# Kernel tuning notes

Hardware: AMD Instinct MI355X
Metric: run time of the kernel (lower is better)

Reference implementation:

```python
import jax, jax.numpy as jnp
import numpy as np

S, N, L = 64, 256, 32
LANG_ID, D = 256, 128  # lang_od == pc_od == D
K = 16  # k; effective neighbors = k+1


def _mlp(x, w1, b1, w2, b2):
    return jnp.maximum(x @ w1 + b1, 0.0) @ w2 + b2


def setup_inputs() -> dict:
    key = jax.random.key(0)
    ks = jax.random.split(key, 16)
    def lin(k, fi, fo):
        return jax.random.normal(k, (fi, fo), jnp.float32) / np.sqrt(fi)
    inp = {
        "feat": jax.random.normal(ks[0], (S, N, D), jnp.float32),
        "coord": jax.random.normal(ks[1], (S, N, 3), jnp.float32),
        "lang_feat": jax.random.normal(ks[2], (S, L, LANG_ID), jnp.float32),
        "lang_len": jax.random.randint(ks[3], (S,), 1, L + 1),
        "rel_w1": lin(ks[4], 10, D), "rel_b1": jnp.zeros((D,), jnp.float32),
        "rel_w2": lin(ks[5], D, D), "rel_b2": jnp.zeros((D,), jnp.float32),
        "lang_w1": lin(ks[6], LANG_ID, D), "lang_b1": jnp.zeros((D,), jnp.float32),
        "lang_w2": lin(ks[7], D, D), "lang_b2": jnp.zeros((D,), jnp.float32),
        "feat_w1": lin(ks[8], D, D), "feat_b1": jnp.zeros((D,), jnp.float32),
        "feat_w2": lin(ks[9], D, D), "feat_b2": jnp.zeros((D,), jnp.float32),
    }
    return inp


def reference(feat, coord, lang_feat, lang_len,
              rel_w1, rel_b1, rel_w2, rel_b2,
              lang_w1, lang_b1, lang_w2, lang_b2,
              feat_w1, feat_b1, feat_w2, feat_b2):
    num_sen, num_obj, _ = feat.shape
    k1 = min(K, num_obj - 1) + 1  # k+1 neighbors including self
    # pairwise squared distances [S,N,N]
    d = ((coord[:, None, :, :] - coord[:, :, None, :]) ** 2).sum(-1)
    # k+1 nearest neighbors (smallest distance)
    _, idx = jax.lax.top_k(-d, k1)  # [S,N,k1]
    b = jnp.arange(num_sen)[:, None, None]
    coord_nb = coord[b, idx]  # [S,N,k1,3]
    coord_ctr = jnp.broadcast_to(coord[:, :, None, :], coord_nb.shape)
    rel_coord = coord_nb - coord_ctr
    dist = jnp.sqrt((rel_coord ** 2).sum(-1, keepdims=True))
    rel = jnp.concatenate([coord_nb, coord_ctr, rel_coord, dist], -1)  # [S,N,k1,10]
    rel = _mlp(rel, rel_w1, rel_b1, rel_w2, rel_b2)  # [S,N,k1,D]
    lang = _mlp(lang_feat, lang_w1, lang_b1, lang_w2, lang_b2)  # [S,L,D]
    f = _mlp(feat, feat_w1, feat_b1, feat_w2, feat_b2)  # [S,N,D]
    f_nb = f[b, idx]  # [S,N,k1,D]
    # attention of each (obj, neighbor) over language tokens
    attn = jnp.einsum('snkd,sld->snkl', f_nb, lang)
    attn = jax.nn.softmax(attn, axis=-1)
    max_len = lang_feat.shape[1]
    mask = (jnp.arange(max_len)[None, :] < lang_len[:, None]).astype(f.dtype)  # [S,L]
    attn = attn * mask[:, None, None, :]
    attn = attn / (attn.sum(-1, keepdims=True) + 1e-7)
    ins = jnp.einsum('snkl,sld->snkd', attn, lang)  # [S,N,k1,D]
    out = (f_nb * ins * rel).sum(2) + f  # [S,N,D]
    score = out.sum(-1)  # [S,N]
    return out, score
```

## Files before the change

### kernel.cpp

```cpp
#include <hip/hip_runtime.h>
#include <math.h>

#define S_ 64
#define N_ 256
#define L_ 32
#define D_ 128
#define LID_ 256
#define K1_ 17
#define CH_ 32
#define NW_ 8

typedef __attribute__((ext_vector_type(8))) short short8;
typedef __attribute__((ext_vector_type(4))) float f32x4;

__device__ __forceinline__ unsigned short f2bf(float f) {
  unsigned int u = __float_as_uint(f);
  u += 0x7fffu + ((u >> 16) & 1u);
  return (unsigned short)(u >> 16);
}


__global__ __launch_bounds__(256) void tar_prep_kernel(
    const float* __restrict__ rw1, const float* __restrict__ rb1,
    const float* __restrict__ rw2, const float* __restrict__ fw1,
    const float* __restrict__ fw2, const float* __restrict__ lw1,
    const float* __restrict__ lw2, unsigned short* __restrict__ w1T,
    unsigned short* __restrict__ w2T, unsigned short* __restrict__ fw1T,
    unsigned short* __restrict__ fw2T, unsigned short* __restrict__ lw1T,
    unsigned short* __restrict__ lw2T) {
  int t = blockIdx.x * 256 + threadIdx.x;
  {
    int k = t >> 7, n = t & 127;
    lw1T[(size_t)n * 256 + k] = f2bf(lw1[(size_t)k * 128 + n]);
  }
  if (t < 16384) {
    int k = t >> 7, n = t & 127;
    int slot =
        32 * (k >> 5) + 8 * ((k & 15) >> 2) + 4 * ((k >> 4) & 1) + (k & 3);
    w2T[(size_t)n * 128 + slot] = f2bf(rw2[(size_t)k * 128 + n]);
    fw1T[(size_t)n * 128 + k] = f2bf(fw1[(size_t)k * 128 + n]);
    fw2T[(size_t)n * 128 + k] = f2bf(fw2[(size_t)k * 128 + n]);
    lw2T[(size_t)n * 128 + k] = f2bf(lw2[(size_t)k * 128 + n]);
  }
  if (t < 2048) {
    int n2 = t >> 4, k2 = t & 15;
    unsigned short v = 0;
    if (k2 < 10) v = f2bf(rw1[(size_t)k2 * 128 + n2]);
    else if (k2 == 10) v = f2bf(rb1[n2]);
    w1T[(size_t)n2 * 16 + k2] = v;
  }
}

#define KNN_NB 1024
#define LANG_NB 32
#define FM_NB 256
__global__ __launch_bounds__(256, 4) void tar_prologue(
    const float* __restrict__ coord, int* __restrict__ idx_out,
    const float* __restrict__ lx, const unsigned short* __restrict__ lw1T,
    const float* __restrict__ lb1, const unsigned short* __restrict__ lw2T,
    const float* __restrict__ lb2, unsigned short* __restrict__ lang_bf,
    unsigned short* __restrict__ langT_bf, const float* __restrict__ fx,
    const unsigned short* __restrict__ fw1T, const float* __restrict__ fb1,
    const unsigned short* __restrict__ fw2T, const float* __restrict__ fb2,
    float* __restrict__ f_out, unsigned short* __restrict__ f_bf) {
  __shared__ __align__(16) char uarena[51200];
  int bid = blockIdx.x;
  int tid = threadIdx.x;

  if (bid < KNN_NB) {
    int wv = tid >> 6, l = tid & 63, grp = l >> 4, ln16 = l & 15;
    int obj = bid * 16 + wv * 4 + grp;
    int s = obj >> 8, n = obj & 255;
    const float* cs = coord + (size_t)s * N_ * 3;
    float cx = cs[n * 3 + 0], cy = cs[n * 3 + 1], cz = cs[n * 3 + 2];
    unsigned kd[16];
#pragma unroll
    for (int q = 0; q < 16; ++q) {
      int j = ln16 + q * 16;
      float dx = cs[j * 3 + 0] - cx;
      float dy = cs[j * 3 + 1] - cy;
      float dz = cs[j * 3 + 2] - cz;
      kd[q] = __float_as_uint(dx * dx + dy * dy + dz * dz);
    }
    for (int k = 0; k < K1_; ++k) {
      unsigned m = kd[0];
#pragma unroll
      for (int q = 1; q < 16; ++q) m = min(m, kd[q]);
      int bq = 0;
#pragma unroll
      for (int q = 15; q >= 0; --q)
        if (kd[q] == m) bq = q;
      int bj = ln16 + bq * 16;
      unsigned bm = m;
#pragma unroll
      for (int off = 1; off <= 8; off <<= 1) {
        unsigned om = __shfl_xor(bm, off);
        int oj = __shfl_xor(bj, off);
        if (om < bm || (om == bm && oj < bj)) { bm = om; bj = oj; }
      }
#pragma unroll
      for (int q = 0; q < 16; ++q)
        if (ln16 + q * 16 == bj) kd[q] = 0xFFFFFFFFu;
      if (ln16 == 0) idx_out[(size_t)obj * K1_ + k] = bj;
    }
  } else if (bid < KNN_NB + LANG_NB) {
    unsigned short* x_s = (unsigned short*)uarena;
    unsigned short* h_s = (unsigned short*)(uarena + 33792);
    int base = (bid - KNN_NB) * 64;
    int w = tid >> 6, l = tid & 63, g = l >> 4, ln = l & 15;
    for (int i = tid; i < 64 * 64; i += 256) {
      int row = i >> 6, c4 = (i & 63) * 4;
      float4 v = *(const float4*)&lx[(size_t)(base + row) * LID_ + c4];
      unsigned short* dst = &x_s[row * 264 + c4];
      dst[0] = f2bf(v.x); dst[1] = f2bf(v.y);
      dst[2] = f2bf(v.z); dst[3] = f2bf(v.w);
    }
    __syncthreads();
    float b1v[8], b2v[8];
#pragma unroll
    for (int nt = 0; nt < 8; ++nt) {
      b1v[nt] = lb1[nt * 16 + ln];
      b2v[nt] = lb2[nt * 16 + ln];
    }
    short8 a1[8];
#pragma unroll
    for (int kk = 0; kk < 8; ++kk)
      a1[kk] = *(const short8*)&x_s[(w * 16 + ln) * 264 + kk * 32 + g * 8];
    unsigned short* hw = &h_s[w * 16 * 136];
#pragma unroll
    for (int nt = 0; nt < 8; ++nt) {
      f32x4 acc = {b1v[nt], b1v[nt], b1v[nt], b1v[nt]};
#pragma unroll
      for (int kk = 0; kk < 8; ++kk) {
        short8 bw =
            *(const short8*)&lw1T[(size_t)(nt * 16 + ln) * 256 + kk * 32 + g * 8];
        acc = __builtin_amdgcn_mfma_f32_16x16x32_bf16(a1[kk], bw, acc, 0, 0, 0);
      }
#pragma unroll
      for (int reg = 0; reg < 4; ++reg)
        hw[(g * 4 + reg) * 136 + nt * 16 + ln] = f2bf(fmaxf(acc[reg], 0.f));
    }
    short8 a2[4];
#pragma unroll
    for (int kk = 0; kk < 4; ++kk)
      a2[kk] = *(const short8*)&hw[ln * 136 + kk * 32 + g * 8];
#pragma unroll
    for (int nt = 0; nt < 8; ++nt) {
      f32x4 acc = {b2v[nt], b2v[nt], b2v[nt], b2v[nt]};
#pragma unroll
      for (int kk = 0; kk < 4; ++kk) {
        short8 bw =
            *(const short8*)&lw2T[(size_t)(nt * 16 + ln) * 128 + kk * 32 + g * 8];
        acc = __builtin_amdgcn_mfma_f32_16x16x32_bf16(a2[kk], bw, acc, 0, 0, 0);
      }
#pragma unroll
      for (int reg = 0; reg < 4; ++reg) {
        int row = base + w * 16 + g * 4 + reg;
        int col = nt * 16 + ln;
        unsigned short hb = f2bf(acc[reg]);
        lang_bf[(size_t)row * D_ + col] = hb;
        int s = row >> 5, t = row & 31;
        int slot = 8 * ((t & 15) >> 2) + 4 * (t >> 4) + (t & 3);
        langT_bf[((size_t)s * D_ + col) * L_ + slot] = hb;
      }
    }
  } else {
    unsigned short* x_s = (unsigned short*)uarena;
    unsigned short* h_s = (unsigned short*)(uarena + 17408);
    int base = (bid - KNN_NB - LANG_NB) * 64;
    int w = tid >> 6, l = tid & 63, g = l >> 4, ln = l & 15;
    for (int i = tid; i < 64 * 32; i += 256) {
      int row = i >> 5, c4 = (i & 31) * 4;
      float4 v = *(const float4*)&fx[(size_t)(base + row) * D_ + c4];
      unsigned short* dst = &x_s[row * 136 + c4];
      dst[0] = f2bf(v.x); dst[1] = f2bf(v.y);
      dst[2] = f2bf(v.z); dst[3] = f2bf(v.w);
    }
    __syncthreads();
    float b1v[8], b2v[8];
#pragma unroll
    for (int nt = 0; nt < 8; ++nt) {
      b1v[nt] = fb1[nt * 16 + ln];
      b2v[nt] = fb2[nt * 16 + ln];
    }
    short8 a1[4];
#pragma unroll
    for (int kk = 0; kk < 4; ++kk)
      a1[kk] = *(const short8*)&x_s[(w * 16 + ln) * 136 + kk * 32 + g * 8];
    unsigned short* hw = &h_s[w * 16 * 136];
#pragma unroll
    for (int nt = 0; nt < 8; ++nt) {
      f32x4 acc = {b1v[nt], b1v[nt], b1v[nt], b1v[nt]};
#pragma unroll
      for (int kk = 0; kk < 4; ++kk) {
        short8 bw =
            *(const short8*)&fw1T[(size_t)(nt * 16 + ln) * 128 + kk * 32 + g * 8];
        acc = __builtin_amdgcn_mfma_f32_16x16x32_bf16(a1[kk], bw, acc, 0, 0, 0);
      }
#pragma unroll
      for (int reg = 0; reg < 4; ++reg)
        hw[(g * 4 + reg) * 136 + nt * 16 + ln] = f2bf(fmaxf(acc[reg], 0.f));
    }
    short8 a2[4];
#pragma unroll
    for (int kk = 0; kk < 4; ++kk)
      a2[kk] = *(const short8*)&hw[ln * 136 + kk * 32 + g * 8];
#pragma unroll
    for (int nt = 0; nt < 8; ++nt) {
      f32x4 acc = {b2v[nt], b2v[nt], b2v[nt], b2v[nt]};
#pragma unroll
      for (int kk = 0; kk < 4; ++kk) {
        short8 bw =
            *(const short8*)&fw2T[(size_t)(nt * 16 + ln) * 128 + kk * 32 + g * 8];
        acc = __builtin_amdgcn_mfma_f32_16x16x32_bf16(a2[kk], bw, acc, 0, 0, 0);
      }
#pragma unroll
      for (int reg = 0; reg < 4; ++reg) {
        int row = base + w * 16 + g * 4 + reg;
        int col = nt * 16 + ln;
        f_out[(size_t)row * D_ + col] = acc[reg];
        f_bf[(size_t)row * D_ + col] = f2bf(acc[reg]);
      }
    }
  }
}

__global__ __launch_bounds__(512, 2) void tar_main_mfma(
    const float* __restrict__ f_out, const unsigned short* __restrict__ f_bf,
    const unsigned short* __restrict__ lang_bf,
    const unsigned short* __restrict__ langT_bf, const int* __restrict__ idxg,
    const float* __restrict__ coord, const unsigned short* __restrict__ w1T_bf,
    const unsigned short* __restrict__ w2T_bf, const float* __restrict__ rel_b2,
    const int* __restrict__ lang_len, float* __restrict__ outp,
    float* __restrict__ score) {
  __shared__ __align__(16) char arena[40960];
  __shared__ float score_s[CH_];

  unsigned short* lang_s = (unsigned short*)(arena);
  unsigned short* langT_s = (unsigned short*)(arena + 8704);
  unsigned short* w1T_s = (unsigned short*)(arena + 18944);
  int* idx_s = (int*)(arena + 25088);

  int b = blockIdx.x;
  int s = b >> 3;
  int chunk = b & 7;
  int sn0 = s * N_ + chunk * CH_;
  int tid = threadIdx.x;
  int w = tid >> 6;
  int l = tid & 63;
  int g = l >> 4;
  int ln = l & 15;
  int og = w >> 2;
  int h = (w >> 1) & 1;
  int q2 = w & 1;
  int len = lang_len[s];

  {
    int row = tid >> 4, c0 = (tid & 15) * 8;
    *(short8*)&lang_s[row * 136 + c0] =
        *(const short8*)&lang_bf[((size_t)s * L_ + row) * D_ + c0];
  }
  {
    int row = tid >> 2, c0 = (tid & 3) * 8;
    *(short8*)&langT_s[row * 40 + c0] =
        *(const short8*)&langT_bf[((size_t)s * D_ + row) * L_ + c0];
  }
  if (tid < 256) {
    int row = tid >> 1, c0 = (tid & 1) * 8;
    *(short8*)&w1T_s[row * 24 + c0] =
        *(const short8*)&w1T_bf[(size_t)row * 16 + c0];
  }
  for (int i = tid; i < CH_ * K1_; i += 512)
    idx_s[i] = idxg[(size_t)sn0 * K1_ + i];
  if (tid < CH_) score_s[tid] = 0.f;
  __syncthreads();

  float b2v[4];
#pragma unroll
  for (int j = 0; j < 4; ++j) b2v[j] = rel_b2[(h * 4 + j) * 16 + ln];

  f32x4 o[4];
#pragma unroll
  for (int j = 0; j < 4; ++j) o[j] = (f32x4){0.f, 0.f, 0.f, 0.f};

  int objA = og * 16 + ln;
  const float* fbase = &f_out[(size_t)s * N_ * D_];
  const float* cA = coord + (size_t)(sn0 + objA) * 3;
  float cx = cA[0], cy = cA[1], cz = cA[2];

  for (int k = q2; k < K1_; k += 2) {
    int nbrA = idx_s[objA * K1_ + k];
    int nbrC[4];
#pragma unroll
    for (int reg = 0; reg < 4; ++reg)
      nbrC[reg] = idx_s[(og * 16 + g * 4 + reg) * K1_ + k];

    const float* cN = coord + (size_t)(s * N_ + nbrA) * 3;
    float nx = cN[0], ny = cN[1], nz = cN[2];
    float rx = nx - cx, ry = ny - cy, rz = nz - cz;
    float dist = sqrtf(rx * rx + ry * ry + rz * rz);
    short8 a1v = {0, 0, 0, 0, 0, 0, 0, 0};
    if (g == 0) {
      a1v[0] = (short)f2bf(nx); a1v[1] = (short)f2bf(ny);
      a1v[2] = (short)f2bf(nz); a1v[3] = (short)f2bf(cx);
      a1v[4] = (short)f2bf(cy); a1v[5] = (short)f2bf(cz);
      a1v[6] = (short)f2bf(rx); a1v[7] = (short)f2bf(ry);
    } else if (g == 1) {
      a1v[0] = (short)f2bf(rz);
      a1v[1] = (short)f2bf(dist);
      a1v[2] = (short)0x3F80;
    }

    const unsigned short* fArow = &f_bf[((size_t)s * N_ + nbrA) * D_];

    f32x4 at0 = {0.f, 0.f, 0.f, 0.f}, at1 = {0.f, 0.f, 0.f, 0.f};
#pragma unroll
    for (int kk = 0; kk < 4; ++kk) {
      short8 fA = *(const short8*)&fArow[kk * 32 + g * 8];
      short8 bb0 = *(const short8*)&lang_s[ln * 136 + kk * 32 + g * 8];
      short8 bb1 = *(const short8*)&lang_s[(16 + ln) * 136 + kk * 32 + g * 8];
      at0 = __builtin_amdgcn_mfma_f32_16x16x32_bf16(bb0, fA, at0, 0, 0, 0);
      at1 = __builtin_amdgcn_mfma_f32_16x16x32_bf16(bb1, fA, at1, 0, 0, 0);
    }

    float mx = fmaxf(fmaxf(fmaxf(at0[0], at0[1]), fmaxf(at0[2], at0[3])),
                     fmaxf(fmaxf(at1[0], at1[1]), fmaxf(at1[2], at1[3])));
    mx = fmaxf(mx, __shfl_xor(mx, 16));
    mx = fmaxf(mx, __shfl_xor(mx, 32));
    float e0[4], e1[4], p0[4], p1[4];
    float ss = 0.f, ms = 0.f;
#pragma unroll
    for (int reg = 0; reg < 4; ++reg) {
      e0[reg] = expf(at0[reg] - mx);
      e1[reg] = expf(at1[reg] - mx);
      ss += e0[reg] + e1[reg];
      p0[reg] = (4 * g + reg < len) ? e0[reg] : 0.f;
      p1[reg] = (16 + 4 * g + reg < len) ? e1[reg] : 0.f;
      ms += p0[reg] + p1[reg];
    }
    ss += __shfl_xor(ss, 16);
    ss += __shfl_xor(ss, 32);
    ms += __shfl_xor(ms, 16);
    ms += __shfl_xor(ms, 32);
    float inv = 1.0f / (ms + 1e-7f * ss);
    short8 pa;
#pragma unroll
    for (int reg = 0; reg < 4; ++reg) {
      pa[reg] = (short)f2bf(p0[reg] * inv);
      pa[4 + reg] = (short)f2bf(p1[reg] * inv);
    }

    short8 a2[4];
#pragma unroll
    for (int kk = 0; kk < 4; ++kk) {
      short8 bw0 = {0, 0, 0, 0, 0, 0, 0, 0};
      short8 bw1 = {0, 0, 0, 0, 0, 0, 0, 0};
      if (g < 2) {
        bw0 = *(const short8*)&w1T_s[((2 * kk) * 16 + ln) * 24 + g * 8];
        bw1 = *(const short8*)&w1T_s[((2 * kk + 1) * 16 + ln) * 24 + g * 8];
      }
      f32x4 z = {0.f, 0.f, 0.f, 0.f};
      f32x4 r0 = __builtin_amdgcn_mfma_f32_16x16x32_bf16(bw0, a1v, z, 0, 0, 0);
      f32x4 r1 = __builtin_amdgcn_mfma_f32_16x16x32_bf16(bw1, a1v, z, 0, 0, 0);
#pragma unroll
      for (int reg = 0; reg < 4; ++reg) {
        a2[kk][reg] = (short)f2bf(fmaxf(r0[reg], 0.f));
        a2[kk][4 + reg] = (short)f2bf(fmaxf(r1[reg], 0.f));
      }
    }

#pragma unroll
    for (int j = 0; j < 4; ++j) {
      int nt = h * 4 + j;
      f32x4 ro = {b2v[j], b2v[j], b2v[j], b2v[j]};
#pragma unroll
      for (int kk = 0; kk < 4; ++kk) {
        short8 bw =
            *(const short8*)&w2T_bf[(size_t)(nt * 16 + ln) * 128 + kk * 32 + g * 8];
        ro = __builtin_amdgcn_mfma_f32_16x16x32_bf16(a2[kk], bw, ro, 0, 0, 0);
      }
      f32x4 iv = {0.f, 0.f, 0.f, 0.f};
      short8 bl = *(const short8*)&langT_s[(nt * 16 + ln) * 40 + g * 8];
      iv = __builtin_amdgcn_mfma_f32_16x16x32_bf16(pa, bl, iv, 0, 0, 0);
#pragma unroll
      for (int reg = 0; reg < 4; ++reg) {
        float fv = fbase[(size_t)nbrC[reg] * D_ + nt * 16 + ln];
        o[j][reg] += fv * iv[reg] * ro[reg];
      }
    }
  }

  __syncthreads();
  float* R = (float*)arena;
  {
    float* Rw = R + w * 1280;
#pragma unroll
    for (int j = 0; j < 4; ++j)
      *(f32x4*)&Rw[(j * 16 + ln) * 20 + g * 4] = o[j];
  }
  __syncthreads();
  {
    int wp = og * 4 + h * 2;
    float vs[2][4];
#pragma unroll
    for (int t = 0; t < 2; ++t) {
      int j = q2 * 2 + t;
      int col = (h * 4 + j) * 16 + ln;
      f32x4 sum = *(f32x4*)&R[wp * 1280 + (j * 16 + ln) * 20 + g * 4];
      sum += *(f32x4*)&R[(wp + 1) * 1280 + (j * 16 + ln) * 20 + g * 4];
#pragma unroll
      for (int reg = 0; reg < 4; ++reg) {
        int obj = og * 16 + g * 4 + reg;
        float v = sum[reg] + f_out[(size_t)(sn0 + obj) * D_ + col];
        outp[(size_t)(sn0 + obj) * D_ + col] = v;
        vs[t][reg] = v;
      }
    }
#pragma unroll
    for (int reg = 0; reg < 4; ++reg) {
      float sv = vs[0][reg] + vs[1][reg];
      sv += __shfl_xor(sv, 1);
      sv += __shfl_xor(sv, 2);
      sv += __shfl_xor(sv, 4);
      sv += __shfl_xor(sv, 8);
      if (ln == 0) atomicAdd(&score_s[og * 16 + g * 4 + reg], sv);
    }
  }
  __syncthreads();
  if (tid < CH_) score[sn0 + tid] = score_s[tid];
}

extern "C" void kernel_launch(void* const* d_in, const int* in_sizes, int n_in,
                              void* d_out, int out_size, void* d_ws,
                              size_t ws_size, hipStream_t stream) {
  const float* feat = (const float*)d_in[0];
  const float* coord = (const float*)d_in[1];
  const float* lang_feat = (const float*)d_in[2];
  const int* lang_len = (const int*)d_in[3];
  const float* rel_w1 = (const float*)d_in[4];
  const float* rel_b1 = (const float*)d_in[5];
  const float* rel_w2 = (const float*)d_in[6];
  const float* rel_b2 = (const float*)d_in[7];
  const float* lang_w1 = (const float*)d_in[8];
  const float* lang_b1 = (const float*)d_in[9];
  const float* lang_w2 = (const float*)d_in[10];
  const float* lang_b2 = (const float*)d_in[11];
  const float* feat_w1 = (const float*)d_in[12];
  const float* feat_b1 = (const float*)d_in[13];
  const float* feat_w2 = (const float*)d_in[14];
  const float* feat_b2 = (const float*)d_in[15];

  char* ws = (char*)d_ws;
  unsigned short* lang_bf = (unsigned short*)(ws);
  unsigned short* langT_bf = (unsigned short*)(ws + 524288);
  float* f_out = (float*)(ws + 1048576);
  unsigned short* f_bf = (unsigned short*)(ws + 9437184);
  int* idx = (int*)(ws + 13631488);
  unsigned short* w2T_bf = (unsigned short*)(ws + 14745600);
  unsigned short* w1T_bf = (unsigned short*)(ws + 14778368);
  unsigned short* fw1T_bf = (unsigned short*)(ws + 14782464);
  unsigned short* fw2T_bf = (unsigned short*)(ws + 14815232);
  unsigned short* lw1T_bf = (unsigned short*)(ws + 14848000);
  unsigned short* lw2T_bf = (unsigned short*)(ws + 14913536);

  float* out = (float*)d_out;
  float* score = out + (size_t)S_ * N_ * D_;

  tar_prep_kernel<<<dim3(128), dim3(256), 0, stream>>>(
      rel_w1, rel_b1, rel_w2, feat_w1, feat_w2, lang_w1, lang_w2, w1T_bf,
      w2T_bf, fw1T_bf, fw2T_bf, lw1T_bf, lw2T_bf);
  tar_prologue<<<dim3(KNN_NB + LANG_NB + FM_NB), dim3(256), 0, stream>>>(
      coord, idx, lang_feat, lw1T_bf, lang_b1, lw2T_bf, lang_b2, lang_bf,
      langT_bf, feat, fw1T_bf, feat_b1, fw2T_bf, feat_b2, f_out, f_bf);
  tar_main_mfma<<<dim3(S_ * (N_ / CH_)), dim3(512), 0, stream>>>(
      f_out, f_bf, lang_bf, langT_bf, idx, coord, w1T_bf, w2T_bf, rel_b2,
      lang_len, out, score);
}
```

Measured before the change: 117.6 us.

## Split neighbor loop across four waves with each wave covering all output tiles

Waves used to split the 8 output column tiles into two halves and the 17 neighbors into two groups. Now each wave computes all 8 column tiles for a quarter of the neighbors. This stops the first-layer relation MLP and attention work from being repeated for each column half. In exchange it doubles the per-wave accumulator and bias registers, which could cause spills under the (512,2) launch bound. It also grows the LDS arena to 64 KB for a four-way cross-wave reduction and leaves the neighbor count unevenly split (5/4/4/4).

Result: slower. 188.6 us (+60.4%).

```diff
diff --git a/kernel.cpp b/kernel.cpp
--- a/kernel.cpp
+++ b/kernel.cpp
@@ -233,7 +233,7 @@
     const unsigned short* __restrict__ w2T_bf, const float* __restrict__ rel_b2,
     const int* __restrict__ lang_len, float* __restrict__ outp,
     float* __restrict__ score) {
-  __shared__ __align__(16) char arena[40960];
+  __shared__ __align__(16) char arena[65536];
   __shared__ float score_s[CH_];
 
   unsigned short* lang_s = (unsigned short*)(arena);
@@ -251,8 +251,7 @@
   int g = l >> 4;
   int ln = l & 15;
   int og = w >> 2;
-  int h = (w >> 1) & 1;
-  int q2 = w & 1;
+  int q = w & 3;
   int len = lang_len[s];
 
   {
@@ -275,20 +274,20 @@
   if (tid < CH_) score_s[tid] = 0.f;
   __syncthreads();
 
-  float b2v[4];
-#pragma unroll
-  for (int j = 0; j < 4; ++j) b2v[j] = rel_b2[(h * 4 + j) * 16 + ln];
-
-  f32x4 o[4];
-#pragma unroll
-  for (int j = 0; j < 4; ++j) o[j] = (f32x4){0.f, 0.f, 0.f, 0.f};
+  float b2v[8];
+#pragma unroll
+  for (int nt = 0; nt < 8; ++nt) b2v[nt] = rel_b2[nt * 16 + ln];
+
+  f32x4 o[8];
+#pragma unroll
+  for (int nt = 0; nt < 8; ++nt) o[nt] = (f32x4){0.f, 0.f, 0.f, 0.f};
 
   int objA = og * 16 + ln;
   const float* fbase = &f_out[(size_t)s * N_ * D_];
   const float* cA = coord + (size_t)(sn0 + objA) * 3;
   float cx = cA[0], cy = cA[1], cz = cA[2];
 
-  for (int k = q2; k < K1_; k += 2) {
+  for (int k = q; k < K1_; k += 4) {
     int nbrA = idx_s[objA * K1_ + k];
     int nbrC[4];
 #pragma unroll
@@ -370,9 +369,8 @@
     }
 
 #pragma unroll
-    for (int j = 0; j < 4; ++j) {
-      int nt = h * 4 + j;
-      f32x4 ro = {b2v[j], b2v[j], b2v[j], b2v[j]};
+    for (int nt = 0; nt < 8; ++nt) {
+      f32x4 ro = {b2v[nt], b2v[nt], b2v[nt], b2v[nt]};
 #pragma unroll
       for (int kk = 0; kk < 4; ++kk) {
         short8 bw =
@@ -385,7 +383,7 @@
 #pragma unroll
       for (int reg = 0; reg < 4; ++reg) {
         float fv = fbase[(size_t)nbrC[reg] * D_ + nt * 16 + ln];
-        o[j][reg] += fv * iv[reg] * ro[reg];
+        o[nt][reg] += fv * iv[reg] * ro[reg];
       }
     }
   }
@@ -393,21 +391,22 @@
   __syncthreads();
   float* R = (float*)arena;
   {
-    float* Rw = R + w * 1280;
-#pragma unroll
-    for (int j = 0; j < 4; ++j)
-      *(f32x4*)&Rw[(j * 16 + ln) * 20 + g * 4] = o[j];
+    float* Rw = R + w * 2048;
+#pragma unroll
+    for (int nt = 0; nt < 8; ++nt)
+      *(f32x4*)&Rw[(nt * 16 + ln) * 16 + g * 4] = o[nt];
   }
   __syncthreads();
   {
-    int wp = og * 4 + h * 2;
     float vs[2][4];
 #pragma unroll
     for (int t = 0; t < 2; ++t) {
-      int j = q2 * 2 + t;
-      int col = (h * 4 + j) * 16 + ln;
-      f32x4 sum = *(f32x4*)&R[wp * 1280 + (j * 16 + ln) * 20 + g * 4];
-      sum += *(f32x4*)&R[(wp + 1) * 1280 + (j * 16 + ln) * 20 + g * 4];
+      int nt = q * 2 + t;
+      int col = nt * 16 + ln;
+      f32x4 sum = {0.f, 0.f, 0.f, 0.f};
+#pragma unroll
+      for (int w2 = 0; w2 < 4; ++w2)
+        sum += *(f32x4*)&R[(og * 4 + w2) * 2048 + col * 16 + g * 4];
 #pragma unroll
       for (int reg = 0; reg < 4; ++reg) {
         int obj = og * 16 + g * 4 + reg;
```

## Fuse KNN neighbor search into main kernel, writing indices directly to shared memory

Applied to the files above, without the earlier changes.

Removes the KNN blocks from the prologue kernel and computes each main block's 32 objects' nearest neighbors inside the main kernel, storing indices in shared memory. This eliminates the global idx buffer write/read and shrinks the prologue grid. In exchange, the main kernel's startup now includes the serial top-k selection before its first barrier, adding latency per block that previously overlapped with the MLP prologue work.

New measurement: 147.5 us. 25.5% more time.

```diff
diff --git a/kernel.cpp b/kernel.cpp
--- a/kernel.cpp
+++ b/kernel.cpp
@@ -51,11 +51,9 @@
   }
 }
 
-#define KNN_NB 1024
 #define LANG_NB 32
 #define FM_NB 256
 __global__ __launch_bounds__(256, 4) void tar_prologue(
-    const float* __restrict__ coord, int* __restrict__ idx_out,
     const float* __restrict__ lx, const unsigned short* __restrict__ lw1T,
     const float* __restrict__ lb1, const unsigned short* __restrict__ lw2T,
     const float* __restrict__ lb2, unsigned short* __restrict__ lang_bf,
@@ -67,46 +65,10 @@
   int bid = blockIdx.x;
   int tid = threadIdx.x;
 
-  if (bid < KNN_NB) {
-    int wv = tid >> 6, l = tid & 63, grp = l >> 4, ln16 = l & 15;
-    int obj = bid * 16 + wv * 4 + grp;
-    int s = obj >> 8, n = obj & 255;
-    const float* cs = coord + (size_t)s * N_ * 3;
-    float cx = cs[n * 3 + 0], cy = cs[n * 3 + 1], cz = cs[n * 3 + 2];
-    unsigned kd[16];
-#pragma unroll
-    for (int q = 0; q < 16; ++q) {
-      int j = ln16 + q * 16;
-      float dx = cs[j * 3 + 0] - cx;
-      float dy = cs[j * 3 + 1] - cy;
-      float dz = cs[j * 3 + 2] - cz;
-      kd[q] = __float_as_uint(dx * dx + dy * dy + dz * dz);
-    }
-    for (int k = 0; k < K1_; ++k) {
-      unsigned m = kd[0];
-#pragma unroll
-      for (int q = 1; q < 16; ++q) m = min(m, kd[q]);
-      int bq = 0;
-#pragma unroll
-      for (int q = 15; q >= 0; --q)
-        if (kd[q] == m) bq = q;
-      int bj = ln16 + bq * 16;
-      unsigned bm = m;
-#pragma unroll
-      for (int off = 1; off <= 8; off <<= 1) {
-        unsigned om = __shfl_xor(bm, off);
-        int oj = __shfl_xor(bj, off);
-        if (om < bm || (om == bm && oj < bj)) { bm = om; bj = oj; }
-      }
-#pragma unroll
-      for (int q = 0; q < 16; ++q)
-        if (ln16 + q * 16 == bj) kd[q] = 0xFFFFFFFFu;
-      if (ln16 == 0) idx_out[(size_t)obj * K1_ + k] = bj;
-    }
-  } else if (bid < KNN_NB + LANG_NB) {
+  if (bid < LANG_NB) {
     unsigned short* x_s = (unsigned short*)uarena;
     unsigned short* h_s = (unsigned short*)(uarena + 33792);
-    int base = (bid - KNN_NB) * 64;
+    int base = bid * 64;
     int w = tid >> 6, l = tid & 63, g = l >> 4, ln = l & 15;
     for (int i = tid; i < 64 * 64; i += 256) {
       int row = i >> 6, c4 = (i & 63) * 4;
@@ -167,7 +129,7 @@
   } else {
     unsigned short* x_s = (unsigned short*)uarena;
     unsigned short* h_s = (unsigned short*)(uarena + 17408);
-    int base = (bid - KNN_NB - LANG_NB) * 64;
+    int base = (bid - LANG_NB) * 64;
     int w = tid >> 6, l = tid & 63, g = l >> 4, ln = l & 15;
     for (int i = tid; i < 64 * 32; i += 256) {
       int row = i >> 5, c4 = (i & 31) * 4;
@@ -228,7 +190,7 @@
 __global__ __launch_bounds__(512, 2) void tar_main_mfma(
     const float* __restrict__ f_out, const unsigned short* __restrict__ f_bf,
     const unsigned short* __restrict__ lang_bf,
-    const unsigned short* __restrict__ langT_bf, const int* __restrict__ idxg,
+    const unsigned short* __restrict__ langT_bf,
     const float* __restrict__ coord, const unsigned short* __restrict__ w1T_bf,
     const unsigned short* __restrict__ w2T_bf, const float* __restrict__ rel_b2,
     const int* __restrict__ lang_len, float* __restrict__ outp,
@@ -270,9 +232,44 @@
     *(short8*)&w1T_s[row * 24 + c0] =
         *(const short8*)&w1T_bf[(size_t)row * 16 + c0];
   }
-  for (int i = tid; i < CH_ * K1_; i += 512)
-    idx_s[i] = idxg[(size_t)sn0 * K1_ + i];
   if (tid < CH_) score_s[tid] = 0.f;
+
+  {
+    int objL = w * 4 + g;
+    int n = chunk * CH_ + objL;
+    const float* cs = coord + (size_t)s * N_ * 3;
+    float cx = cs[n * 3 + 0], cy = cs[n * 3 + 1], cz = cs[n * 3 + 2];
+    unsigned kd[16];
+#pragma unroll
+    for (int q = 0; q < 16; ++q) {
+      int j = ln + q * 16;
+      float dx = cs[j * 3 + 0] - cx;
+      float dy = cs[j * 3 + 1] - cy;
+      float dz = cs[j * 3 + 2] - cz;
+      kd[q] = __float_as_uint(dx * dx + dy * dy + dz * dz);
+    }
+    for (int k = 0; k < K1_; ++k) {
+      unsigned m = kd[0];
+#pragma unroll
+      for (int q = 1; q < 16; ++q) m = min(m, kd[q]);
+      int bq = 0;
+#pragma unroll
+      for (int q = 15; q >= 0; --q)
+        if (kd[q] == m) bq = q;
+      int bj = ln + bq * 16;
+      unsigned bm = m;
+#pragma unroll
+      for (int off = 1; off <= 8; off <<= 1) {
+        unsigned om = __shfl_xor(bm, off);
+        int oj = __shfl_xor(bj, off);
+        if (om < bm || (om == bm && oj < bj)) { bm = om; bj = oj; }
+      }
+#pragma unroll
+      for (int q = 0; q < 16; ++q)
+        if (ln + q * 16 == bj) kd[q] = 0xFFFFFFFFu;
+      if (ln == 0) idx_s[objL * K1_ + k] = bj;
+    }
+  }
   __syncthreads();
 
   float b2v[4];
@@ -455,7 +452,6 @@
   unsigned short* langT_bf = (unsigned short*)(ws + 524288);
   float* f_out = (float*)(ws + 1048576);
   unsigned short* f_bf = (unsigned short*)(ws + 9437184);
-  int* idx = (int*)(ws + 13631488);
   unsigned short* w2T_bf = (unsigned short*)(ws + 14745600);
   unsigned short* w1T_bf = (unsigned short*)(ws + 14778368);
   unsigned short* fw1T_bf = (unsigned short*)(ws + 14782464);
@@ -469,10 +465,10 @@
   tar_prep_kernel<<<dim3(128), dim3(256), 0, stream>>>(
       rel_w1, rel_b1, rel_w2, feat_w1, feat_w2, lang_w1, lang_w2, w1T_bf,
       w2T_bf, fw1T_bf, fw2T_bf, lw1T_bf, lw2T_bf);
-  tar_prologue<<<dim3(KNN_NB + LANG_NB + FM_NB), dim3(256), 0, stream>>>(
-      coord, idx, lang_feat, lw1T_bf, lang_b1, lw2T_bf, lang_b2, lang_bf,
-      langT_bf, feat, fw1T_bf, feat_b1, fw2T_bf, feat_b2, f_out, f_bf);
+  tar_prologue<<<dim3(LANG_NB + FM_NB), dim3(256), 0, stream>>>(
+      lang_feat, lw1T_bf, lang_b1, lw2T_bf, lang_b2, lang_bf, langT_bf, feat,
+      fw1T_bf, feat_b1, fw2T_bf, feat_b2, f_out, f_bf);
   tar_main_mfma<<<dim3(S_ * (N_ / CH_)), dim3(512), 0, stream>>>(
-      f_out, f_bf, lang_bf, langT_bf, idx, coord, w1T_bf, w2T_bf, rel_b2,
-      lang_len, out, score);
+      f_out, f_bf, lang_bf, langT_bf, coord, w1T_bf, w2T_bf, rel_b2, lang_len,
+      out, score);
 }
```
